# Kernel optimization log

Hardware: AMD Instinct MI355X
Metric: run time of the kernel (lower is better)

Reference implementation:

```python
import jax, jax.numpy as jnp
import numpy as np

N_NODES = 50000
N_EDGES = 1_600_000
DIMS = [512, 2048, 1024, 512]  # input, hiddens..., output
NEG_SLOPE = 0.2
EPS = 1e-12


def setup_inputs() -> dict:
    key = jax.random.key(0)
    ks = jax.random.split(key, 12)
    inp = {
        "x": jax.random.normal(ks[0], (N_NODES, DIMS[0]), dtype=jnp.float32),
        "edge_row": jax.random.randint(ks[1], (N_EDGES,), 0, N_NODES, dtype=jnp.int32),
        "edge_col": jax.random.randint(ks[2], (N_EDGES,), 0, N_NODES, dtype=jnp.int32),
        "edge_val": jax.random.uniform(ks[3], (N_EDGES,), dtype=jnp.float32),
    }
    # GraphConvolution params per layer: W [d_in, d_out], b [d_out]
    for i in range(len(DIMS) - 1):
        d_in, d_out = DIMS[i], DIMS[i + 1]
        scale = 1.0 / np.sqrt(d_in)
        inp[f"W{i}"] = jax.random.uniform(ks[4 + 2 * i], (d_in, d_out), minval=-scale, maxval=scale, dtype=jnp.float32)
        inp[f"b{i}"] = jnp.zeros((d_out,), dtype=jnp.float32)
    return inp


def _spmm(edge_row, edge_col, edge_val, h):
    # out[i] = sum_{e: row[e]==i} val[e] * h[col[e]]   (sparse adj @ h)
    msgs = edge_val[:, None] * h[edge_col]  # [E, d]
    return jax.ops.segment_sum(msgs, edge_row, num_segments=N_NODES)


def reference(x, edge_row, edge_col, edge_val, W0, b0, W1, b1, W2, b2):
    Ws = [W0, W1, W2]
    bs = [b0, b1, b2]
    # F.normalize: L2-normalize each row
    norm = jnp.sqrt(jnp.sum(x * x, axis=1, keepdims=True))
    h = x / jnp.maximum(norm, EPS)
    n_layers = len(Ws)
    for i in range(n_layers):
        support = h @ Ws[i]                                  # [N, d_out]
        h = _spmm(edge_row, edge_col, edge_val, support) + bs[i]
        if i != n_layers - 1:
            # dropout is identity at inference; leaky_relu(0.2)
            h = jnp.where(h >= 0, h, NEG_SLOPE * h)
    return h
```

## Files before the change

### kernel.cpp

```cpp
#include <hip/hip_runtime.h>
#include <stdint.h>

#define N_NODES 50000
#define N_EDGES 1600000

typedef __attribute__((ext_vector_type(8))) short bf16x8;
typedef __attribute__((ext_vector_type(4))) float f32x4;
typedef __attribute__((ext_vector_type(8))) unsigned short u16x8;

__device__ __forceinline__ float b2f(unsigned short u) {
  union { unsigned int i; float f; } v; v.i = ((unsigned int)u) << 16; return v.f;
}
__device__ __forceinline__ unsigned short f2b(float f) {
  union { float f; unsigned int i; } v; v.f = f;
  unsigned int u = v.i;
  u += 0x7fffu + ((u >> 16) & 1u);
  return (unsigned short)(u >> 16);
}

__device__ __forceinline__ void load_lds16(const void* g, void* l) {
  __builtin_amdgcn_global_load_lds(
      (const __attribute__((address_space(1))) unsigned int*)g,
      (__attribute__((address_space(3))) unsigned int*)l, 16, 0, 0);
}

__global__ __launch_bounds__(256) void normalize_k(const float* __restrict__ x,
                                                   unsigned short* __restrict__ out) {
  int lane = threadIdx.x & 63;
  int row = blockIdx.x * 4 + (threadIdx.x >> 6);
  const float* p = x + (size_t)row * 512 + lane * 8;
  float4 a = ((const float4*)p)[0];
  float4 b = ((const float4*)p)[1];
  float ss = a.x*a.x + a.y*a.y + a.z*a.z + a.w*a.w
           + b.x*b.x + b.y*b.y + b.z*b.z + b.w*b.w;
#pragma unroll
  for (int off = 1; off < 64; off <<= 1) ss += __shfl_xor(ss, off, 64);
  float s = 1.0f / fmaxf(sqrtf(ss), 1e-12f);
  u16x8 o;
  o[0]=f2b(a.x*s); o[1]=f2b(a.y*s); o[2]=f2b(a.z*s); o[3]=f2b(a.w*s);
  o[4]=f2b(b.x*s); o[5]=f2b(b.y*s); o[6]=f2b(b.z*s); o[7]=f2b(b.w*s);
  *(u16x8*)(out + (size_t)row * 512 + lane * 8) = o;
}

__global__ __launch_bounds__(256) void hist_k(const int* __restrict__ er, int* __restrict__ deg) {
  int i = blockIdx.x * 256 + threadIdx.x;
  if (i < N_EDGES) atomicAdd(&deg[er[i]], 1);
}

__global__ __launch_bounds__(256) void scan1_k(const int* __restrict__ deg, int* __restrict__ out,
                                               int* __restrict__ csum, int n) {
  __shared__ int sd[256];
  int t = threadIdx.x;
  int base = blockIdx.x * 1024;
  int v[4], s = 0;
#pragma unroll
  for (int j = 0; j < 4; ++j) {
    int idx = base + t * 4 + j;
    v[j] = (idx < n) ? deg[idx] : 0;
    s += v[j];
  }
  sd[t] = s;
  __syncthreads();
  for (int off = 1; off < 256; off <<= 1) {
    int xx = (t >= off) ? sd[t - off] : 0;
    __syncthreads();
    sd[t] += xx;
    __syncthreads();
  }
  if (t == 255) csum[blockIdx.x] = sd[255];
  int run = sd[t] - s;
#pragma unroll
  for (int j = 0; j < 4; ++j) {
    int idx = base + t * 4 + j;
    if (idx < n) out[idx] = run;
    run += v[j];
  }
}

__global__ void scan2_k(int* csum, int n) {
  if (threadIdx.x == 0 && blockIdx.x == 0) {
    int s = 0;
    for (int i = 0; i < n; ++i) { int t = csum[i]; csum[i] = s; s += t; }
  }
}

__global__ __launch_bounds__(256) void scan3_k(int* __restrict__ out, const int* __restrict__ csum, int n) {
  int i = blockIdx.x * 256 + threadIdx.x;
  if (i < n) out[i] += csum[i >> 10];
}

__global__ __launch_bounds__(256) void scatter_k(const int* __restrict__ er, const int* __restrict__ ec,
    const float* __restrict__ ev, int* __restrict__ head, int2* __restrict__ ep) {
  int i = blockIdx.x * 256 + threadIdx.x;
  if (i < N_EDGES) {
    int r = er[i];
    int p = atomicAdd(&head[r], 1);
    ep[p] = make_int2(ec[i], __float_as_int(ev[i]));
  }
}

__global__ __launch_bounds__(256) void wconv_k(const float* __restrict__ W,
                                               unsigned short* __restrict__ WT, int K, int N) {
  int i = blockIdx.x * 256 + threadIdx.x;
  if (i < N * K) {
    int n = i / K, k = i - n * K;
    WT[i] = f2b(W[(size_t)k * N + n]);
  }
}

template <int D, int MODE>
__global__ __launch_bounds__(256) void spmm_k(const unsigned short* __restrict__ in,
    const int* __restrict__ rs, const int2* __restrict__ ep,
    const float* __restrict__ bias, void* __restrict__ outv) {
  constexpr int NS = D / 512;
  int lane = threadIdx.x & 63;
  int blk = blockIdx.x;
  int slice = (NS == 1) ? 0 : (blk / 12500);
  int rowg = (NS == 1) ? blk : (blk - slice * 12500);
  int row = rowg * 4 + (threadIdx.x >> 6);
  int e0 = rs[row];
  int e1 = (row + 1 == N_NODES) ? N_EDGES : rs[row + 1];
  float acc[8] = {0.f, 0.f, 0.f, 0.f, 0.f, 0.f, 0.f, 0.f};
  const unsigned short* base = in + (size_t)slice * 512 + (size_t)lane * 8;
  int e = e0;
  for (; e + 4 <= e1; e += 4) {
    int2 p0 = ep[e];
    int2 p1 = ep[e + 1];
    int2 p2 = ep[e + 2];
    int2 p3 = ep[e + 3];
    u16x8 u0 = *(const u16x8*)(base + (size_t)p0.x * D);
    u16x8 u1 = *(const u16x8*)(base + (size_t)p1.x * D);
    u16x8 u2 = *(const u16x8*)(base + (size_t)p2.x * D);
    u16x8 u3 = *(const u16x8*)(base + (size_t)p3.x * D);
    float v0 = __int_as_float(p0.y), v1 = __int_as_float(p1.y);
    float v2 = __int_as_float(p2.y), v3 = __int_as_float(p3.y);
#pragma unroll
    for (int h = 0; h < 8; ++h) acc[h] = fmaf(v0, b2f(u0[h]), acc[h]);
#pragma unroll
    for (int h = 0; h < 8; ++h) acc[h] = fmaf(v1, b2f(u1[h]), acc[h]);
#pragma unroll
    for (int h = 0; h < 8; ++h) acc[h] = fmaf(v2, b2f(u2[h]), acc[h]);
#pragma unroll
    for (int h = 0; h < 8; ++h) acc[h] = fmaf(v3, b2f(u3[h]), acc[h]);
  }
  for (; e < e1; ++e) {
    int2 p = ep[e];
    u16x8 u = *(const u16x8*)(base + (size_t)p.x * D);
    float v = __int_as_float(p.y);
#pragma unroll
    for (int h = 0; h < 8; ++h) acc[h] = fmaf(v, b2f(u[h]), acc[h]);
  }
  size_t obase = (size_t)row * D + (size_t)slice * 512 + lane * 8;
  int bbase = slice * 512 + lane * 8;
  if (MODE == 2) {
    float* out = (float*)outv;
#pragma unroll
    for (int j = 0; j < 8; ++j) out[obase + j] = acc[j] + bias[bbase + j];
  } else {
    unsigned short* out = (unsigned short*)outv;
    u16x8 o;
#pragma unroll
    for (int h = 0; h < 8; ++h) {
      float xo = acc[h];
      if (MODE == 1) {
        xo += bias[bbase + h];
        xo = xo >= 0.f ? xo : 0.2f * xo;
      }
      o[h] = f2b(xo);
    }
    *(u16x8*)(out + obase) = o;
  }
}

template <bool BIAS_RELU>
__global__ __launch_bounds__(256) void gemm_bt_k(
    const unsigned short* __restrict__ A, const unsigned short* __restrict__ BT,
    const float* __restrict__ bias, unsigned short* __restrict__ C,
    int M, int N, int K) {
  __shared__ __align__(16) unsigned short sA[128 * 32];
  __shared__ __align__(16) unsigned short sB[128 * 32];
  int tid = threadIdx.x;
  int lane = tid & 63;
  int wid = tid >> 6;
  int wm = (wid & 1) * 64;
  int wn = (wid >> 1) * 64;
  int mblk = blockIdx.y * 128;
  int nblk = blockIdx.x * 128;
  const unsigned short* Bb = BT + (size_t)nblk * K;
  int c0 = tid, c1 = tid + 256;
  int ar0 = c0 >> 2, ac0 = (c0 & 3) * 8;
  int ar1 = c1 >> 2, ac1 = (c1 & 3) * 8;
  int ra0 = mblk + ar0; if (ra0 > M - 1) ra0 = M - 1;
  int ra1 = mblk + ar1; if (ra1 > M - 1) ra1 = M - 1;
  f32x4 acc[4][4] = {};
  for (int k0 = 0; k0 < K; k0 += 32) {
    load_lds16(A + (size_t)ra0 * K + k0 + ac0, &sA[c0 * 8]);
    load_lds16(A + (size_t)ra1 * K + k0 + ac1, &sA[c1 * 8]);
    load_lds16(Bb + (size_t)ar0 * K + k0 + ac0, &sB[c0 * 8]);
    load_lds16(Bb + (size_t)ar1 * K + k0 + ac1, &sB[c1 * 8]);
    __syncthreads();
    bf16x8 af[4], bfr[4];
    int kq = (lane >> 4) * 8;
    int mr = wm + (lane & 15);
    int nr = wn + (lane & 15);
#pragma unroll
    for (int i = 0; i < 4; ++i) af[i] = *(const bf16x8*)&sA[(mr + i * 16) * 32 + kq];
#pragma unroll
    for (int j = 0; j < 4; ++j) bfr[j] = *(const bf16x8*)&sB[(nr + j * 16) * 32 + kq];
#pragma unroll
    for (int i = 0; i < 4; ++i)
#pragma unroll
      for (int j = 0; j < 4; ++j)
        acc[i][j] = __builtin_amdgcn_mfma_f32_16x16x32_bf16(af[i], bfr[j], acc[i][j], 0, 0, 0);
    __syncthreads();
  }
  int quad = lane >> 4;
  int lc = lane & 15;
#pragma unroll
  for (int i = 0; i < 4; ++i) {
#pragma unroll
    for (int r = 0; r < 4; ++r) {
      int gm = mblk + wm + i * 16 + quad * 4 + r;
      if (gm < M) {
#pragma unroll
        for (int j = 0; j < 4; ++j) {
          int gn = nblk + wn + j * 16 + lc;
          float v = acc[i][j][r];
          if (BIAS_RELU) { v += bias[gn]; v = v >= 0.f ? v : 0.2f * v; }
          C[(size_t)gm * N + gn] = f2b(v);
        }
      }
    }
  }
}

extern "C" void kernel_launch(void* const* d_in, const int* in_sizes, int n_in,
                              void* d_out, int out_size, void* d_ws, size_t ws_size,
                              hipStream_t stream) {
  (void)in_sizes; (void)n_in; (void)out_size; (void)ws_size;
  const float* x  = (const float*)d_in[0];
  const int* erow = (const int*)d_in[1];
  const int* ecol = (const int*)d_in[2];
  const float* ev = (const float*)d_in[3];
  const float* W0 = (const float*)d_in[4];
  const float* b0 = (const float*)d_in[5];
  const float* W1 = (const float*)d_in[6];
  const float* b1 = (const float*)d_in[7];
  const float* W2 = (const float*)d_in[8];
  const float* b2 = (const float*)d_in[9];

  char* ws = (char*)d_ws;
  unsigned short* norm_out  = (unsigned short*)(ws);
  unsigned short* spmm0_out = (unsigned short*)(ws + 51200000);
  unsigned short* h1chunk   = (unsigned short*)(ws + 102400000);
  unsigned short* h2        = (unsigned short*)(ws);
  unsigned short* vbuf      = (unsigned short*)(ws + 102400000);
  int2*  ep   = (int2*)(ws + 153600000);
  int*   rs   = (int*)(ws + 166400000);
  int*   head = (int*)(ws + 166600192);
  int*   deg  = (int*)(ws + 166800384);
  int*   csum = (int*)(ws + 167000576);
  unsigned short* w0t = (unsigned short*)(ws + 167000832);
  unsigned short* w1t = w0t + (size_t)2048 * 512;
  unsigned short* w2t = w1t + (size_t)1024 * 2048;
  unsigned short* u   = (unsigned short*)d_out;

  hipMemsetAsync(deg, 0, N_NODES * 4, stream);
  hist_k<<<6250, 256, 0, stream>>>(erow, deg);
  scan1_k<<<49, 256, 0, stream>>>(deg, rs, csum, N_NODES);
  scan2_k<<<1, 64, 0, stream>>>(csum, 49);
  scan3_k<<<196, 256, 0, stream>>>(rs, csum, N_NODES);
  hipMemcpyAsync(head, rs, N_NODES * 4, hipMemcpyDeviceToDevice, stream);
  scatter_k<<<6250, 256, 0, stream>>>(erow, ecol, ev, head, ep);

  wconv_k<<<4096, 256, 0, stream>>>(W0, w0t, 512, 2048);
  wconv_k<<<8192, 256, 0, stream>>>(W1, w1t, 2048, 1024);
  wconv_k<<<2048, 256, 0, stream>>>(W2, w2t, 1024, 512);

  normalize_k<<<12500, 256, 0, stream>>>(x, norm_out);

  spmm_k<512, 0><<<12500, 256, 0, stream>>>(norm_out, rs, ep, nullptr, spmm0_out);

  for (int c = 0; c < 4; ++c) {
    const unsigned short* a0 = spmm0_out + (size_t)c * 12500 * 512;
    unsigned short* uc = u + (size_t)c * 12500 * 1024;
    gemm_bt_k<true ><<<dim3(16, 98), 256, 0, stream>>>(a0, w0t, b0, h1chunk, 12500, 2048, 512);
    gemm_bt_k<false><<<dim3(8, 98), 256, 0, stream>>>(h1chunk, w1t, nullptr, uc, 12500, 1024, 2048);
  }

  spmm_k<1024, 1><<<25000, 256, 0, stream>>>(u, rs, ep, b1, h2);

  gemm_bt_k<false><<<dim3(4, 391), 256, 0, stream>>>(h2, w2t, nullptr, vbuf, N_NODES, 512, 1024);
  spmm_k<512, 2><<<12500, 256, 0, stream>>>(vbuf, rs, ep, b2, (float*)d_out);
}
```

Before: 2.034 ms.

## Sort CSR edges by column bucket and unchunk GEMMs when workspace allows

Builds the CSR with a two-level key (row, column>>12) so each row's edges are grouped by source-column bucket, aiming for better cache locality in the SpMM gathers. Replaces the serial second-level scan with a parallel block scan and clamps column indices. Adds workspace-size tiers so the first two GEMMs run over all 50000 rows at once (or in two chunks) instead of four, cutting launch count and tail waste. The bucketed histogram and scan are 13x larger, which adds preprocessing cost.

```diff
diff --git a/kernel.cpp b/kernel.cpp
--- a/kernel.cpp
+++ b/kernel.cpp
@@ -3,6 +3,7 @@
 
 #define N_NODES 50000
 #define N_EDGES 1600000
+#define NCB 13
 
 typedef __attribute__((ext_vector_type(8))) short bf16x8;
 typedef __attribute__((ext_vector_type(4))) float f32x4;
@@ -42,9 +43,10 @@
   *(u16x8*)(out + (size_t)row * 512 + lane * 8) = o;
 }
 
-__global__ __launch_bounds__(256) void hist_k(const int* __restrict__ er, int* __restrict__ deg) {
-  int i = blockIdx.x * 256 + threadIdx.x;
-  if (i < N_EDGES) atomicAdd(&deg[er[i]], 1);
+__global__ __launch_bounds__(256) void hist2_k(const int* __restrict__ er, const int* __restrict__ ec,
+                                               int* __restrict__ h2) {
+  int i = blockIdx.x * 256 + threadIdx.x;
+  if (i < N_EDGES) atomicAdd(&h2[er[i] * NCB + (ec[i] >> 12)], 1);
 }
 
 __global__ __launch_bounds__(256) void scan1_k(const int* __restrict__ deg, int* __restrict__ out,
@@ -77,10 +79,30 @@
   }
 }
 
-__global__ void scan2_k(int* csum, int n) {
-  if (threadIdx.x == 0 && blockIdx.x == 0) {
-    int s = 0;
-    for (int i = 0; i < n; ++i) { int t = csum[i]; csum[i] = s; s += t; }
+__global__ __launch_bounds__(256) void scan2p_k(int* __restrict__ csum, int n) {
+  __shared__ int sd[256];
+  int t = threadIdx.x;
+  int v[3], s = 0;
+#pragma unroll
+  for (int j = 0; j < 3; ++j) {
+    int idx = t * 3 + j;
+    v[j] = (idx < n) ? csum[idx] : 0;
+    s += v[j];
+  }
+  sd[t] = s;
+  __syncthreads();
+  for (int off = 1; off < 256; off <<= 1) {
+    int xx = (t >= off) ? sd[t - off] : 0;
+    __syncthreads();
+    sd[t] += xx;
+    __syncthreads();
+  }
+  int run = sd[t] - s;
+#pragma unroll
+  for (int j = 0; j < 3; ++j) {
+    int idx = t * 3 + j;
+    if (idx < n) csum[idx] = run;
+    run += v[j];
   }
 }
 
@@ -89,13 +111,19 @@
   if (i < n) out[i] += csum[i >> 10];
 }
 
-__global__ __launch_bounds__(256) void scatter_k(const int* __restrict__ er, const int* __restrict__ ec,
-    const float* __restrict__ ev, int* __restrict__ head, int2* __restrict__ ep) {
+__global__ __launch_bounds__(256) void extract_k(const int* __restrict__ rs2, int* __restrict__ rs_s) {
+  int i = blockIdx.x * 256 + threadIdx.x;
+  if (i < N_NODES) rs_s[i] = rs2[i * NCB];
+  if (i == N_NODES) rs_s[i] = N_EDGES;
+}
+
+__global__ __launch_bounds__(256) void scatter2_k(const int* __restrict__ er, const int* __restrict__ ec,
+    const float* __restrict__ ev, int* __restrict__ head2, int2* __restrict__ ep) {
   int i = blockIdx.x * 256 + threadIdx.x;
   if (i < N_EDGES) {
-    int r = er[i];
-    int p = atomicAdd(&head[r], 1);
-    ep[p] = make_int2(ec[i], __float_as_int(ev[i]));
+    int r = er[i], c = ec[i];
+    int p = atomicAdd(&head2[r * NCB + (c >> 12)], 1);
+    ep[p] = make_int2(c, __float_as_int(ev[i]));
   }
 }
 
@@ -119,7 +147,7 @@
   int rowg = (NS == 1) ? blk : (blk - slice * 12500);
   int row = rowg * 4 + (threadIdx.x >> 6);
   int e0 = rs[row];
-  int e1 = (row + 1 == N_NODES) ? N_EDGES : rs[row + 1];
+  int e1 = rs[row + 1];
   float acc[8] = {0.f, 0.f, 0.f, 0.f, 0.f, 0.f, 0.f, 0.f};
   const unsigned short* base = in + (size_t)slice * 512 + (size_t)lane * 8;
   int e = e0;
@@ -128,10 +156,14 @@
     int2 p1 = ep[e + 1];
     int2 p2 = ep[e + 2];
     int2 p3 = ep[e + 3];
-    u16x8 u0 = *(const u16x8*)(base + (size_t)p0.x * D);
-    u16x8 u1 = *(const u16x8*)(base + (size_t)p1.x * D);
-    u16x8 u2 = *(const u16x8*)(base + (size_t)p2.x * D);
-    u16x8 u3 = *(const u16x8*)(base + (size_t)p3.x * D);
+    unsigned c0 = (unsigned)p0.x < N_NODES ? (unsigned)p0.x : 0u;
+    unsigned c1 = (unsigned)p1.x < N_NODES ? (unsigned)p1.x : 0u;
+    unsigned c2 = (unsigned)p2.x < N_NODES ? (unsigned)p2.x : 0u;
+    unsigned c3 = (unsigned)p3.x < N_NODES ? (unsigned)p3.x : 0u;
+    u16x8 u0 = *(const u16x8*)(base + (size_t)c0 * D);
+    u16x8 u1 = *(const u16x8*)(base + (size_t)c1 * D);
+    u16x8 u2 = *(const u16x8*)(base + (size_t)c2 * D);
+    u16x8 u3 = *(const u16x8*)(base + (size_t)c3 * D);
     float v0 = __int_as_float(p0.y), v1 = __int_as_float(p1.y);
     float v2 = __int_as_float(p2.y), v3 = __int_as_float(p3.y);
 #pragma unroll
@@ -145,7 +177,8 @@
   }
   for (; e < e1; ++e) {
     int2 p = ep[e];
-    u16x8 u = *(const u16x8*)(base + (size_t)p.x * D);
+    unsigned c = (unsigned)p.x < N_NODES ? (unsigned)p.x : 0u;
+    u16x8 u = *(const u16x8*)(base + (size_t)c * D);
     float v = __int_as_float(p.y);
 #pragma unroll
     for (int h = 0; h < 8; ++h) acc[h] = fmaf(v, b2f(u[h]), acc[h]);
@@ -237,7 +270,7 @@
 extern "C" void kernel_launch(void* const* d_in, const int* in_sizes, int n_in,
                               void* d_out, int out_size, void* d_ws, size_t ws_size,
                               hipStream_t stream) {
-  (void)in_sizes; (void)n_in; (void)out_size; (void)ws_size;
+  (void)in_sizes; (void)n_in; (void)out_size;
   const float* x  = (const float*)d_in[0];
   const int* erow = (const int*)d_in[1];
   const int* ecol = (const int*)d_in[2];
@@ -249,47 +282,69 @@
   const float* W2 = (const float*)d_in[8];
   const float* b2 = (const float*)d_in[9];
 
+  const size_t POOL_T1 = 256000000;
+  const size_t POOL_T2 = 204800000;
+  const size_t POOL_T3 = 153600000;
+  const size_t META = 12800000 + 200064 + 7340032;
+  int tier = (ws_size >= POOL_T1 + META) ? 1 : (ws_size >= POOL_T2 + META) ? 2 : 3;
+  size_t pool_sz = (tier == 1) ? POOL_T1 : (tier == 2) ? POOL_T2 : POOL_T3;
+
   char* ws = (char*)d_ws;
-  unsigned short* norm_out  = (unsigned short*)(ws);
-  unsigned short* spmm0_out = (unsigned short*)(ws + 51200000);
-  unsigned short* h1chunk   = (unsigned short*)(ws + 102400000);
-  unsigned short* h2        = (unsigned short*)(ws);
-  unsigned short* vbuf      = (unsigned short*)(ws + 102400000);
-  int2*  ep   = (int2*)(ws + 153600000);
-  int*   rs   = (int*)(ws + 166400000);
-  int*   head = (int*)(ws + 166600192);
-  int*   deg  = (int*)(ws + 166800384);
-  int*   csum = (int*)(ws + 167000576);
-  unsigned short* w0t = (unsigned short*)(ws + 167000832);
+  int2*  ep   = (int2*)(ws + pool_sz);
+  int*   rs_s = (int*)(ws + pool_sz + 12800000);
+  unsigned short* w0t = (unsigned short*)(ws + pool_sz + 12800000 + 200064);
   unsigned short* w1t = w0t + (size_t)2048 * 512;
   unsigned short* w2t = w1t + (size_t)1024 * 2048;
-  unsigned short* u   = (unsigned short*)d_out;
-
-  hipMemsetAsync(deg, 0, N_NODES * 4, stream);
-  hist_k<<<6250, 256, 0, stream>>>(erow, deg);
-  scan1_k<<<49, 256, 0, stream>>>(deg, rs, csum, N_NODES);
-  scan2_k<<<1, 64, 0, stream>>>(csum, 49);
-  scan3_k<<<196, 256, 0, stream>>>(rs, csum, N_NODES);
-  hipMemcpyAsync(head, rs, N_NODES * 4, hipMemcpyDeviceToDevice, stream);
-  scatter_k<<<6250, 256, 0, stream>>>(erow, ecol, ev, head, ep);
+  int* rs2   = (int*)(ws);
+  int* csum  = (int*)(ws + 2600064);
+  int* head2 = (int*)(ws + 2604160);
+  unsigned short* u = (unsigned short*)d_out;
+
+  hipMemsetAsync(rs2, 0, 2600064, stream);
+  hist2_k<<<6250, 256, 0, stream>>>(erow, ecol, rs2);
+  scan1_k<<<635, 256, 0, stream>>>(rs2, rs2, csum, N_NODES * NCB);
+  scan2p_k<<<1, 256, 0, stream>>>(csum, 635);
+  scan3_k<<<2540, 256, 0, stream>>>(rs2, csum, N_NODES * NCB);
+  extract_k<<<196, 256, 0, stream>>>(rs2, rs_s);
+  hipMemcpyAsync(head2, rs2, (size_t)N_NODES * NCB * 4, hipMemcpyDeviceToDevice, stream);
+  scatter2_k<<<6250, 256, 0, stream>>>(erow, ecol, ev, head2, ep);
 
   wconv_k<<<4096, 256, 0, stream>>>(W0, w0t, 512, 2048);
   wconv_k<<<8192, 256, 0, stream>>>(W1, w1t, 2048, 1024);
   wconv_k<<<2048, 256, 0, stream>>>(W2, w2t, 1024, 512);
 
-  normalize_k<<<12500, 256, 0, stream>>>(x, norm_out);
-
-  spmm_k<512, 0><<<12500, 256, 0, stream>>>(norm_out, rs, ep, nullptr, spmm0_out);
-
-  for (int c = 0; c < 4; ++c) {
-    const unsigned short* a0 = spmm0_out + (size_t)c * 12500 * 512;
-    unsigned short* uc = u + (size_t)c * 12500 * 1024;
-    gemm_bt_k<true ><<<dim3(16, 98), 256, 0, stream>>>(a0, w0t, b0, h1chunk, 12500, 2048, 512);
-    gemm_bt_k<false><<<dim3(8, 98), 256, 0, stream>>>(h1chunk, w1t, nullptr, uc, 12500, 1024, 2048);
-  }
-
-  spmm_k<1024, 1><<<25000, 256, 0, stream>>>(u, rs, ep, b1, h2);
-
-  gemm_bt_k<false><<<dim3(4, 391), 256, 0, stream>>>(h2, w2t, nullptr, vbuf, N_NODES, 512, 1024);
-  spmm_k<512, 2><<<12500, 256, 0, stream>>>(vbuf, rs, ep, b2, (float*)d_out);
-}
+  if (tier == 1) {
+    unsigned short* h1        = (unsigned short*)(ws);
+    unsigned short* norm_out  = (unsigned short*)(ws);
+    unsigned short* spmm0_out = (unsigned short*)(ws + 204800000);
+    unsigned short* h2        = (unsigned short*)(ws);
+    unsigned short* vbuf      = (unsigned short*)(ws + 102400000);
+    normalize_k<<<12500, 256, 0, stream>>>(x, norm_out);
+    spmm_k<512, 0><<<12500, 256, 0, stream>>>(norm_out, rs_s, ep, nullptr, spmm0_out);
+    gemm_bt_k<true ><<<dim3(16, 391), 256, 0, stream>>>(spmm0_out, w0t, b0, h1, N_NODES, 2048, 512);
+    gemm_bt_k<false><<<dim3(8, 391), 256, 0, stream>>>(h1, w1t, nullptr, u, N_NODES, 1024, 2048);
+    spmm_k<1024, 1><<<25000, 256, 0, stream>>>(u, rs_s, ep, b1, h2);
+    gemm_bt_k<false><<<dim3(4, 391), 256, 0, stream>>>(h2, w2t, nullptr, vbuf, N_NODES, 512, 1024);
+    spmm_k<512, 2><<<12500, 256, 0, stream>>>(vbuf, rs_s, ep, b2, (float*)d_out);
+  } else {
+    int nchunk = (tier == 2) ? 2 : 4;
+    int crows = (tier == 2) ? 25000 : 12500;
+    int ytiles = (tier == 2) ? 196 : 98;
+    unsigned short* norm_out  = (unsigned short*)(ws);
+    unsigned short* spmm0_out = (unsigned short*)(ws + 51200000);
+    unsigned short* h1chunk   = (unsigned short*)(ws + 102400000);
+    unsigned short* h2        = (unsigned short*)(ws);
+    unsigned short* vbuf      = (unsigned short*)(ws + 102400000);
+    normalize_k<<<12500, 256, 0, stream>>>(x, norm_out);
+    spmm_k<512, 0><<<12500, 256, 0, stream>>>(norm_out, rs_s, ep, nullptr, spmm0_out);
+    for (int c = 0; c < nchunk; ++c) {
+      const unsigned short* a0 = spmm0_out + (size_t)c * crows * 512;
+      unsigned short* uc = u + (size_t)c * crows * 1024;
+      gemm_bt_k<true ><<<dim3(16, ytiles), 256, 0, stream>>>(a0, w0t, b0, h1chunk, crows, 2048, 512);
+      gemm_bt_k<false><<<dim3(8, ytiles), 256, 0, stream>>>(h1chunk, w1t, nullptr, uc, crows, 1024, 2048);
+    }
+    spmm_k<1024, 1><<<25000, 256, 0, stream>>>(u, rs_s, ep, b1, h2);
+    gemm_bt_k<false><<<dim3(4, 391), 256, 0, stream>>>(h2, w2t, nullptr, vbuf, N_NODES, 512, 1024);
+    spmm_k<512, 2><<<12500, 256, 0, stream>>>(vbuf, rs_s, ep, b2, (float*)d_out);
+  }
+}
```

Result: faster. 1.850 ms (-9.1%).
